# Optimization experiments

Measured on AMD Instinct MI355X. Metric: run time of the kernel, lower is better.

Reference implementation:

```python
import jax, jax.numpy as jnp
import numpy as np
import math

H = 16  # n_head
DK = 64  # d_k = n_feat // n_head
BASE = 10000.0


def _rope_cos_sin(T, dk, dtype):
    inv_freq = 1.0 / (BASE ** (jnp.arange(0, dk, 2, dtype=jnp.float32) / dk))
    t = jnp.arange(T, dtype=jnp.float32)
    freqs = jnp.einsum('i,j->ij', t, inv_freq)          # [T, dk/2]
    emb = jnp.concatenate([freqs, freqs], axis=-1)       # [T, dk]
    return jnp.cos(emb).astype(dtype)[:, None, None, :], jnp.sin(emb).astype(dtype)[:, None, None, :]


def _rotate_half(x):
    x1, x2 = jnp.split(x, 2, axis=-1)
    return jnp.concatenate([-x2, x1], axis=-1)


def setup_inputs() -> dict:
    key = jax.random.key(0)
    ks = jax.random.split(key, 8)
    T, B, C = 2048, 2, 1024
    s = 0.02
    return {
        'query': jax.random.normal(ks[0], (T, B, C), jnp.float32),
        'key': jax.random.normal(ks[1], (T, B, C), jnp.float32),
        'value': jax.random.normal(ks[2], (T, B, C), jnp.float32),
        'Wq': jax.random.normal(ks[3], (C, C), jnp.float32) * s,
        'bq': jnp.zeros((C,), jnp.float32),
        'Wk': jax.random.normal(ks[4], (C, C), jnp.float32) * s,
        'bk': jnp.zeros((C,), jnp.float32),
        'Wv': jax.random.normal(ks[5], (C, C), jnp.float32) * s,
        'bv': jnp.zeros((C,), jnp.float32),
        'Wo': jax.random.normal(ks[6], (C, C), jnp.float32) * s,
        'bo': jnp.zeros((C,), jnp.float32),
    }


def reference(query, key, value, Wq, bq, Wk, bk, Wv, bv, Wo, bo):
    T, B, C = value.shape
    # --- RoPE applied to raw inputs (per the original module), before projections ---
    q = query.reshape(T, B, H, DK)
    k = key.reshape(T, B, H, DK)
    cos, sin = _rope_cos_sin(T, DK, q.dtype)  # [T,1,1,DK]
    q = q * cos + _rotate_half(q) * sin
    k = k * cos + _rotate_half(k) * sin
    q = q.reshape(T, B, C).transpose(1, 0, 2)   # [B,T,C]
    k = k.reshape(T, B, C).transpose(1, 0, 2)
    v = value.transpose(1, 0, 2)
    # --- QKV projections (torch Linear: x @ W.T + b) ---
    q = (jnp.einsum('btc,dc->btd', q, Wq) + bq).reshape(B, T, H, DK).transpose(0, 2, 1, 3)
    k = (jnp.einsum('btc,dc->btd', k, Wk) + bk).reshape(B, T, H, DK).transpose(0, 2, 1, 3)
    v = (jnp.einsum('btc,dc->btd', v, Wv) + bv).reshape(B, T, H, DK).transpose(0, 2, 1, 3)
    # --- scaled dot-product attention ---
    scores = jnp.einsum('bhqd,bhkd->bhqk', q, k) / math.sqrt(DK)
    attn = jax.nn.softmax(scores, axis=-1)
    x = jnp.einsum('bhqk,bhkd->bhqd', attn, v)        # [B,H,T,DK]
    x = x.transpose(0, 2, 1, 3).reshape(B, T, C)
    out = jnp.einsum('btc,dc->btd', x, Wo) + bo        # [B,T,C]
    return out.transpose(1, 0, 2)                      # [T,B,C]
```

## Files before the change

### kernel.cpp

```cpp
#include <hip/hip_runtime.h>
#include <hip/hip_bf16.h>
#include <math.h>

#define T_SEQ 2048
#define B_SZ 2
#define C_DIM 1024
#define H_HEADS 16
#define DKH 64
#define M_ROWS (T_SEQ * B_SZ)

#define QSCALE 0.1803368801111204f

typedef __attribute__((ext_vector_type(8))) short bf16x8;
typedef __attribute__((ext_vector_type(4))) float f32x4;
typedef unsigned short ushort_t;


__device__ __forceinline__ ushort_t f2bf(float f) {
    unsigned u = __float_as_uint(f);
    u += 0x7fffu + ((u >> 16) & 1u);
    return (ushort_t)(u >> 16);
}

__device__ __forceinline__ unsigned pack2bf(float a, float b) {
#if __has_builtin(__builtin_amdgcn_cvt_pk_bf16_f32)
    typedef __attribute__((ext_vector_type(2))) __bf16 bf16x2_t;
    union { bf16x2_t v; unsigned u; } cv;
    cv.v = __builtin_amdgcn_cvt_pk_bf16_f32(a, b);
    return cv.u;
#else
    return (unsigned)f2bf(a) | ((unsigned)f2bf(b) << 16);
#endif
}

__device__ __forceinline__ void async_copy16(const void* g, void* l) {
    __builtin_amdgcn_global_load_lds(
        (const __attribute__((address_space(1))) void*)g,
        (__attribute__((address_space(3))) void*)l, 16, 0, 0);
}

__global__ __launch_bounds__(256) void prep_all(
        const float* __restrict__ q, const float* __restrict__ k,
        const float* __restrict__ value,
        const float* __restrict__ Wq, const float* __restrict__ Wk,
        const float* __restrict__ Wv, const float* __restrict__ Wo,
        ushort_t* __restrict__ qb, ushort_t* __restrict__ kb,
        ushort_t* __restrict__ vb2,
        ushort_t* __restrict__ Wqb, ushort_t* __restrict__ Wkb,
        ushort_t* __restrict__ Wvb, ushort_t* __restrict__ Wob) {
    int bid = blockIdx.x;
    int tid = threadIdx.x;
    if (bid < 8192) {
        int idx  = bid * 256 + tid;
        int j    = idx & 31;
        int rest = idx >> 5;
        int h    = rest & (H_HEADS - 1);
        int tb   = rest >> 4;
        int t    = tb >> 1;
        float inv = exp2f(-(float)j * 0.41524101186092034f);
        float ang = (float)t * inv;
        float s, c;
        sincosf(ang, &s, &c);
        int base = tb * C_DIM + h * DKH + j;
        float q1 = q[base], q2 = q[base + 32];
        float k1 = k[base], k2 = k[base + 32];
        qb[base]      = f2bf(q1 * c - q2 * s);
        qb[base + 32] = f2bf(q2 * c + q1 * s);
        kb[base]      = f2bf(k1 * c - k2 * s);
        kb[base + 32] = f2bf(k2 * c + k1 * s);
    } else if (bid < 12288) {
        int i   = (bid - 8192) * 256 + tid;
        int c4  = i & 255;
        int row = i >> 8;
        int b   = row >> 11, t = row & 2047;
        float4 v = reinterpret_cast<const float4*>(value)[(t * 2 + b) * 256 + c4];
        ushort4 o;
        o.x = f2bf(v.x); o.y = f2bf(v.y); o.z = f2bf(v.z); o.w = f2bf(v.w);
        reinterpret_cast<ushort4*>(vb2)[i] = o;
    } else {
        int r     = bid - 12288;
        int which = r >> 10;
        int i     = (r & 1023) * 256 + tid;
        const float* in = which == 0 ? Wq : which == 1 ? Wk : which == 2 ? Wv : Wo;
        ushort_t*   out = which == 0 ? Wqb : which == 1 ? Wkb : which == 2 ? Wvb : Wob;
        float4 v = reinterpret_cast<const float4*>(in)[i];
        ushort4 o;
        o.x = f2bf(v.x); o.y = f2bf(v.y); o.z = f2bf(v.z); o.w = f2bf(v.w);
        reinterpret_cast<ushort4*>(out)[i] = o;
    }
}

__device__ __forceinline__ void gemm_core(
        ushort_t* AsBase, ushort_t* BsBase,
        const ushort_t* __restrict__ A, const ushort_t* __restrict__ W,
        const float* __restrict__ bias, void* __restrict__ Cout,
        int N, int K, float scale, int rowBase, int colBase,
        bool biasRow, bool bf16out) {
    const int tid  = threadIdx.x;
    const int lane = tid & 63;
    const int w    = tid >> 6;
    const int m16  = lane & 15, quad = lane >> 4;
    const int r8   = lane >> 3, c8 = lane & 7;
    const int clog = c8 ^ r8;

    f32x4 acc[4];
#pragma unroll
    for (int j = 0; j < 4; j++) acc[j] = (f32x4){0.f, 0.f, 0.f, 0.f};

    auto stage = [&](int buf, int kt) {
#pragma unroll
        for (int i = 0; i < 2; ++i) {
            int R = w * 16 + i * 8;
            async_copy16(A + (size_t)(rowBase + R + r8) * K + kt + clog * 8,
                         AsBase + buf * 8192 + R * 64);
        }
        {
            int R = w * 8;
            async_copy16(W + (size_t)(colBase + R + r8) * K + kt + clog * 8,
                         BsBase + buf * 4096 + R * 64);
        }
    };

    stage(0, 0);
    int cur = 0;
    for (int kt = 0; kt < K; kt += 64, cur ^= 1) {
        if (kt + 64 < K) {
            stage(cur ^ 1, kt + 64);
            asm volatile("s_waitcnt vmcnt(3)" ::: "memory");
        } else {
            asm volatile("s_waitcnt vmcnt(0)" ::: "memory");
        }
        __builtin_amdgcn_s_barrier();
        __builtin_amdgcn_sched_barrier(0);
        const ushort_t* Asc = AsBase + cur * 8192;
        const ushort_t* Bsc = BsBase + cur * 4096;
#pragma unroll
        for (int ks = 0; ks < 2; ++ks) {
            int lc = ks * 4 + quad;
            bf16x8 af;
            {
                int R = w * 16 + m16;
                af = *reinterpret_cast<const bf16x8*>(
                    &Asc[R * 64 + ((lc ^ (R & 7)) << 3)]);
            }
            bf16x8 bfr[4];
#pragma unroll
            for (int ni = 0; ni < 4; ni++) {
                int R = ni * 16 + m16;
                bfr[ni] = *reinterpret_cast<const bf16x8*>(
                    &Bsc[R * 64 + ((lc ^ (R & 7)) << 3)]);
            }
#pragma unroll
            for (int ni = 0; ni < 4; ni++)
                acc[ni] = __builtin_amdgcn_mfma_f32_16x16x32_bf16(
                    af, bfr[ni], acc[ni], 0, 0, 0);
        }
        __builtin_amdgcn_s_barrier();
    }
#pragma unroll
    for (int ni = 0; ni < 4; ni++)
#pragma unroll
        for (int r = 0; r < 4; r++) {
            int row = rowBase + w * 16 + quad * 4 + r;
            int col = colBase + ni * 16 + m16;
            float v = (acc[ni][r] + (biasRow ? bias[row] : bias[col])) * scale;
            if (bf16out)
                ((ushort_t*)Cout)[(size_t)row * N + col] = f2bf(v);
            else
                ((float*)Cout)[(size_t)row * N + col] = v;
        }
}

__global__ __launch_bounds__(512) void qkv_gemm(
        const ushort_t* __restrict__ qb, const ushort_t* __restrict__ kb,
        const ushort_t* __restrict__ Wqb, const ushort_t* __restrict__ Wkb,
        const ushort_t* __restrict__ Wvb, const ushort_t* __restrict__ vb2,
        const float* __restrict__ bq, const float* __restrict__ bk,
        const float* __restrict__ bv,
        ushort_t* __restrict__ Qp, ushort_t* __restrict__ Kp,
        ushort_t* __restrict__ VTg) {
    __shared__ ushort_t As[2][128 * 64];
    __shared__ ushort_t Bs[2][64 * 64];
    int z = blockIdx.y;
    const ushort_t* A; const ushort_t* W; const float* bias; ushort_t* C;
    int N, bx, by; bool biasRow; float scale;
    if (z == 0) {
        A = qb;  W = Wqb; bias = bq; C = Qp;  N = C_DIM;  biasRow = false;
        scale = QSCALE; bx = blockIdx.x & 15; by = blockIdx.x >> 4;
    } else if (z == 1) {
        A = kb;  W = Wkb; bias = bk; C = Kp;  N = C_DIM;  biasRow = false;
        scale = 1.0f;   bx = blockIdx.x & 15; by = blockIdx.x >> 4;
    } else {
        A = Wvb; W = vb2; bias = bv; C = VTg; N = M_ROWS; biasRow = true;
        scale = 1.0f;   bx = blockIdx.x & 63; by = blockIdx.x >> 6;
    }
    gemm_core(&As[0][0], &Bs[0][0], A, W, bias, C, N, C_DIM, scale,
              by * 128, bx * 64, biasRow, true);
}

__global__ __launch_bounds__(512) void gemm_o(
        const ushort_t* __restrict__ Xb, const ushort_t* __restrict__ Wob,
        const float* __restrict__ bo, float* __restrict__ out) {
    __shared__ ushort_t As[2][128 * 64];
    __shared__ ushort_t Bs[2][64 * 64];
    gemm_core(&As[0][0], &Bs[0][0], Xb, Wob, bo, out, C_DIM, C_DIM, 1.0f,
              blockIdx.y * 128, blockIdx.x * 64, false, false);
}

__global__ __launch_bounds__(256) void attn(
        const ushort_t* __restrict__ Qp, const ushort_t* __restrict__ Kp,
        const ushort_t* __restrict__ VTg, ushort_t* __restrict__ X) {
    __shared__ char smem[40960];
    ushort_t* Qt = (ushort_t*)smem;
    char*  KtC   = smem + 8192;
    char*  VTC   = smem + 24576;
    float* exch  = (float*)(smem + 8192);
    float* lbuf  = (float*)smem;

    const int tid  = threadIdx.x;
    const int lane = tid & 63;
    const int w    = tid >> 6;
    const int m16  = lane & 15, quad = lane >> 4;
    const int r8   = lane >> 3, c8 = lane & 7;
    const int clog = c8 ^ r8;

    const int lid   = blockIdx.x + blockIdx.y * 32;
    const int jj    = lid >> 3;
    const int pair  = (lid & 7) * 4 + (jj >> 5);
    const int qBase = (jj & 31) * 64;
    const int b = pair >> 4, h = pair & 15;

    const int ofA = m16 * 128 + ((quad ^ (m16 & 7)) << 4);
    const int ofB = m16 * 128 + (((4 + quad) ^ (m16 & 7)) << 4);
    const int sw4 = (m16 >> 1) & 3;
    const int fro = m16 * 64 + ((quad ^ sw4) << 4);
    int pw0[2];
#pragma unroll
    for (int kt_i = 0; kt_i < 2; kt_i++)
        pw0[kt_i] = m16 * 64 + (((kt_i * 2 + (quad >> 1)) ^ sw4) << 4) + (quad & 1) * 8;
    char* PwC = KtC + w * 4096;

    const int vlc = (lane & 3) ^ ((lane >> 3) & 3);

#pragma unroll
    for (int i = 0; i < 2; ++i) {
        int R = w * 16 + i * 8;
        async_copy16(Qp + (size_t)((qBase + R + r8) * 2 + b) * C_DIM + h * DKH + clog * 8,
                     &Qt[R * 64]);
    }
    __syncthreads();
    bf16x8 aq[4][2];
#pragma unroll
    for (int ni = 0; ni < 4; ni++) {
        aq[ni][0] = *reinterpret_cast<const bf16x8*>((const char*)Qt + ni * 2048 + ofA);
        aq[ni][1] = *reinterpret_cast<const bf16x8*>((const char*)Qt + ni * 2048 + ofB);
    }
    asm volatile("s_waitcnt lgkmcnt(0)" ::: "memory");
    __syncthreads();

    float lrun[4] = {0.f, 0.f, 0.f, 0.f};
    f32x4 o[4][4];
#pragma unroll
    for (int mi = 0; mi < 4; mi++)
#pragma unroll
        for (int ni = 0; ni < 4; ni++) o[mi][ni] = (f32x4){0.f, 0.f, 0.f, 0.f};

    auto stageKV = [&](int kt) {
#pragma unroll
        for (int i = 0; i < 4; ++i) {
            int key = kt + w * 32 + i * 8 + r8;
            async_copy16(Kp + (size_t)(key * 2 + b) * C_DIM + h * DKH + clog * 8,
                         KtC + w * 4096 + i * 1024);
        }
#pragma unroll
        for (int i = 0; i < 4; ++i) {
            int dkr = i * 16 + (lane >> 2);
            async_copy16(VTg + (size_t)(h * DKH + dkr) * M_ROWS + b * T_SEQ + kt + w * 32 + vlc * 8,
                         VTC + w * 4096 + i * 1024);
        }
    };

    stageKV(0);
    for (int kt = 0; kt < T_SEQ; kt += 128) {
        asm volatile("s_waitcnt vmcnt(0)" ::: "memory");
        __builtin_amdgcn_sched_barrier(0);

        f32x4 s[2][4];
#pragma unroll
        for (int kt_i = 0; kt_i < 2; kt_i++) {
#pragma unroll
            for (int ni = 0; ni < 4; ni++) s[kt_i][ni] = (f32x4){0.f, 0.f, 0.f, 0.f};
            bf16x8 kf0 = *reinterpret_cast<const bf16x8*>(KtC + w * 4096 + kt_i * 2048 + ofA);
            bf16x8 kf1 = *reinterpret_cast<const bf16x8*>(KtC + w * 4096 + kt_i * 2048 + ofB);
#pragma unroll
            for (int ni = 0; ni < 4; ni++) {
                s[kt_i][ni] = __builtin_amdgcn_mfma_f32_16x16x32_bf16(kf0, aq[ni][0], s[kt_i][ni], 0, 0, 0);
                s[kt_i][ni] = __builtin_amdgcn_mfma_f32_16x16x32_bf16(kf1, aq[ni][1], s[kt_i][ni], 0, 0, 0);
            }
        }

#pragma unroll
        for (int kt_i = 0; kt_i < 2; kt_i++)
#pragma unroll
            for (int ni = 0; ni < 4; ni++) {
                float p0 = __builtin_amdgcn_exp2f(s[kt_i][ni][0]);
                float p1 = __builtin_amdgcn_exp2f(s[kt_i][ni][1]);
                float p2 = __builtin_amdgcn_exp2f(s[kt_i][ni][2]);
                float p3 = __builtin_amdgcn_exp2f(s[kt_i][ni][3]);
                lrun[ni] += (p0 + p1) + (p2 + p3);
                uint2 pv;
                pv.x = pack2bf(p0, p1);
                pv.y = pack2bf(p2, p3);
                *reinterpret_cast<uint2*>(PwC + ni * 1024 + pw0[kt_i]) = pv;
            }
        asm volatile("s_waitcnt lgkmcnt(0)" ::: "memory");

        bf16x8 pf[4];
#pragma unroll
        for (int ni = 0; ni < 4; ni++)
            pf[ni] = *reinterpret_cast<const bf16x8*>(PwC + ni * 1024 + fro);
        bf16x8 vfr[4];
#pragma unroll
        for (int mi = 0; mi < 4; mi++)
            vfr[mi] = *reinterpret_cast<const bf16x8*>(VTC + w * 4096 + mi * 1024 + fro);
        asm volatile("s_waitcnt lgkmcnt(0)" ::: "memory");
        __builtin_amdgcn_sched_barrier(0);
        if (kt + 128 < T_SEQ) stageKV(kt + 128);
        __builtin_amdgcn_sched_barrier(0);

#pragma unroll
        for (int mi = 0; mi < 4; mi++)
#pragma unroll
            for (int ni = 0; ni < 4; ni++)
                o[mi][ni] = __builtin_amdgcn_mfma_f32_16x16x32_bf16(vfr[mi], pf[ni], o[mi][ni], 0, 0, 0);
    }

#pragma unroll
    for (int ni = 0; ni < 4; ni++) {
        lrun[ni] += __shfl_xor(lrun[ni], 16);
        lrun[ni] += __shfl_xor(lrun[ni], 32);
    }
    float lv = quad == 0 ? lrun[0] : quad == 1 ? lrun[1] : quad == 2 ? lrun[2] : lrun[3];
    lbuf[w * 64 + quad * 16 + m16] = lv;

    __syncthreads();

#pragma unroll
    for (int rnd = 0; rnd < 2; rnd++) {
        if (rnd) __syncthreads();
#pragma unroll
        for (int t2 = 0; t2 < 2; t2++) {
            int mi = 2 * rnd + t2;
#pragma unroll
            for (int ni = 0; ni < 4; ni++) {
                int q = ni * 16 + m16;
                int cw = t2 * 4 + quad;
                *reinterpret_cast<f32x4*>(
                    &exch[w * 2048 + q * 32 + ((cw ^ (q & 7)) << 2)]) = o[mi][ni];
            }
        }
        __syncthreads();
        int q = tid >> 2;
        float lsum = lbuf[q] + lbuf[64 + q] + lbuf[128 + q] + lbuf[192 + q];
        float invl = 1.0f / lsum;
#pragma unroll
        for (int half = 0; half < 2; half++) {
            int c = (tid & 3) + 4 * half;
            int off = q * 32 + (((c ^ (q & 7))) << 2);
            f32x4 v = *reinterpret_cast<const f32x4*>(&exch[off]);
            f32x4 v1 = *reinterpret_cast<const f32x4*>(&exch[2048 + off]);
            f32x4 v2 = *reinterpret_cast<const f32x4*>(&exch[4096 + off]);
            f32x4 v3 = *reinterpret_cast<const f32x4*>(&exch[6144 + off]);
            v = v + v1 + v2 + v3;
            uint2 pk;
            pk.x = pack2bf(v[0] * invl, v[1] * invl);
            pk.y = pack2bf(v[2] * invl, v[3] * invl);
            int t = qBase + q;
            *reinterpret_cast<uint2*>(
                &X[(size_t)(t * 2 + b) * C_DIM + h * DKH + rnd * 32 + c * 4]) = pk;
        }
    }
}

extern "C" void kernel_launch(void* const* d_in, const int* in_sizes, int n_in,
                              void* d_out, int out_size, void* d_ws, size_t ws_size,
                              hipStream_t stream) {
    const float* query = (const float*)d_in[0];
    const float* key   = (const float*)d_in[1];
    const float* value = (const float*)d_in[2];
    const float* Wq = (const float*)d_in[3];
    const float* bq = (const float*)d_in[4];
    const float* Wk = (const float*)d_in[5];
    const float* bk = (const float*)d_in[6];
    const float* Wv = (const float*)d_in[7];
    const float* bv = (const float*)d_in[8];
    const float* Wo = (const float*)d_in[9];
    const float* bo = (const float*)d_in[10];
    float* out = (float*)d_out;

    ushort_t* qb  = (ushort_t*)d_ws;
    ushort_t* kb  = qb  + (size_t)M_ROWS * C_DIM;
    ushort_t* vb2 = kb  + (size_t)M_ROWS * C_DIM;
    ushort_t* Wqb = vb2 + (size_t)M_ROWS * C_DIM;
    ushort_t* Wkb = Wqb + (size_t)C_DIM * C_DIM;
    ushort_t* Wvb = Wkb + (size_t)C_DIM * C_DIM;
    ushort_t* Wob = Wvb + (size_t)C_DIM * C_DIM;
    ushort_t* Qp  = Wob + (size_t)C_DIM * C_DIM;
    ushort_t* Kp  = Qp  + (size_t)M_ROWS * C_DIM;
    ushort_t* VTg = Kp  + (size_t)M_ROWS * C_DIM;
    ushort_t* Xb  = VTg + (size_t)M_ROWS * C_DIM;

    prep_all<<<16384, 256, 0, stream>>>(query, key, value, Wq, Wk, Wv, Wo,
                                        qb, kb, vb2, Wqb, Wkb, Wvb, Wob);

    qkv_gemm<<<dim3(512, 3), 512, 0, stream>>>(qb, kb, Wqb, Wkb, Wvb, vb2,
                                               bq, bk, bv, Qp, Kp, VTg);

    attn<<<dim3(T_SEQ / 64, B_SZ * H_HEADS), 256, 0, stream>>>(Qp, Kp, VTg, Xb);

    gemm_o<<<dim3(C_DIM / 64, M_ROWS / 128), 512, 0, stream>>>(Xb, Wob, bo, out);
}
```

Measured before the change: 225.6 us.

## Switch GEMMs to 128x128 tiles with 4x4 MFMA per wave, drop double buffering

The shared GEMM core now uses 256-thread blocks computing 128x128 output tiles, where each wave computes a 64x64 sub-tile with a 4x4 grid of MFMA accumulators. Before, 512-thread blocks produced 128x64 tiles. Each fragment loaded from LDS now feeds more MFMAs, which raises data reuse and cuts global and LDS traffic per flop. In exchange, the async double-buffered prefetch is replaced by a single buffer with __syncthreads, so load latency is no longer overlapped with compute. The grids also shrink by half, which may reduce occupancy on a large GPU.

```diff
diff --git a/kernel.cpp b/kernel.cpp
--- a/kernel.cpp
+++ b/kernel.cpp
@@ -91,7 +91,7 @@
 }
 
 __device__ __forceinline__ void gemm_core(
-        ushort_t* AsBase, ushort_t* BsBase,
+        ushort_t* As, ushort_t* Bs,
         const ushort_t* __restrict__ A, const ushort_t* __restrict__ W,
         const float* __restrict__ bias, void* __restrict__ Cout,
         int N, int K, float scale, int rowBase, int colBase,
@@ -99,79 +99,75 @@
     const int tid  = threadIdx.x;
     const int lane = tid & 63;
     const int w    = tid >> 6;
+    const int wr   = (w >> 1) * 64;
+    const int wc   = (w & 1) * 64;
     const int m16  = lane & 15, quad = lane >> 4;
     const int r8   = lane >> 3, c8 = lane & 7;
     const int clog = c8 ^ r8;
 
-    f32x4 acc[4];
-#pragma unroll
-    for (int j = 0; j < 4; j++) acc[j] = (f32x4){0.f, 0.f, 0.f, 0.f};
-
-    auto stage = [&](int buf, int kt) {
-#pragma unroll
-        for (int i = 0; i < 2; ++i) {
-            int R = w * 16 + i * 8;
+    f32x4 acc[4][4];
+#pragma unroll
+    for (int mi = 0; mi < 4; mi++)
+#pragma unroll
+        for (int ni = 0; ni < 4; ni++) acc[mi][ni] = (f32x4){0.f, 0.f, 0.f, 0.f};
+
+    for (int kt = 0; kt < K; kt += 64) {
+#pragma unroll
+        for (int i = 0; i < 4; ++i) {
+            int R = w * 32 + i * 8;
             async_copy16(A + (size_t)(rowBase + R + r8) * K + kt + clog * 8,
-                         AsBase + buf * 8192 + R * 64);
-        }
-        {
-            int R = w * 8;
+                         As + R * 64);
+        }
+#pragma unroll
+        for (int i = 0; i < 4; ++i) {
+            int R = w * 32 + i * 8;
             async_copy16(W + (size_t)(colBase + R + r8) * K + kt + clog * 8,
-                         BsBase + buf * 4096 + R * 64);
-        }
-    };
-
-    stage(0, 0);
-    int cur = 0;
-    for (int kt = 0; kt < K; kt += 64, cur ^= 1) {
-        if (kt + 64 < K) {
-            stage(cur ^ 1, kt + 64);
-            asm volatile("s_waitcnt vmcnt(3)" ::: "memory");
-        } else {
-            asm volatile("s_waitcnt vmcnt(0)" ::: "memory");
-        }
-        __builtin_amdgcn_s_barrier();
-        __builtin_amdgcn_sched_barrier(0);
-        const ushort_t* Asc = AsBase + cur * 8192;
-        const ushort_t* Bsc = BsBase + cur * 4096;
+                         Bs + R * 64);
+        }
+        __syncthreads();
 #pragma unroll
         for (int ks = 0; ks < 2; ++ks) {
             int lc = ks * 4 + quad;
-            bf16x8 af;
-            {
-                int R = w * 16 + m16;
-                af = *reinterpret_cast<const bf16x8*>(
-                    &Asc[R * 64 + ((lc ^ (R & 7)) << 3)]);
+            bf16x8 af[4];
+#pragma unroll
+            for (int mi = 0; mi < 4; mi++) {
+                int R = wr + mi * 16 + m16;
+                af[mi] = *reinterpret_cast<const bf16x8*>(
+                    &As[R * 64 + ((lc ^ (R & 7)) << 3)]);
             }
             bf16x8 bfr[4];
 #pragma unroll
             for (int ni = 0; ni < 4; ni++) {
-                int R = ni * 16 + m16;
+                int R = wc + ni * 16 + m16;
                 bfr[ni] = *reinterpret_cast<const bf16x8*>(
-                    &Bsc[R * 64 + ((lc ^ (R & 7)) << 3)]);
-            }
-#pragma unroll
-            for (int ni = 0; ni < 4; ni++)
-                acc[ni] = __builtin_amdgcn_mfma_f32_16x16x32_bf16(
-                    af, bfr[ni], acc[ni], 0, 0, 0);
-        }
-        __builtin_amdgcn_s_barrier();
-    }
-#pragma unroll
-    for (int ni = 0; ni < 4; ni++)
-#pragma unroll
-        for (int r = 0; r < 4; r++) {
-            int row = rowBase + w * 16 + quad * 4 + r;
-            int col = colBase + ni * 16 + m16;
-            float v = (acc[ni][r] + (biasRow ? bias[row] : bias[col])) * scale;
-            if (bf16out)
-                ((ushort_t*)Cout)[(size_t)row * N + col] = f2bf(v);
-            else
-                ((float*)Cout)[(size_t)row * N + col] = v;
-        }
-}
-
-__global__ __launch_bounds__(512) void qkv_gemm(
+                    &Bs[R * 64 + ((lc ^ (R & 7)) << 3)]);
+            }
+#pragma unroll
+            for (int mi = 0; mi < 4; mi++)
+#pragma unroll
+                for (int ni = 0; ni < 4; ni++)
+                    acc[mi][ni] = __builtin_amdgcn_mfma_f32_16x16x32_bf16(
+                        af[mi], bfr[ni], acc[mi][ni], 0, 0, 0);
+        }
+        __syncthreads();
+    }
+#pragma unroll
+    for (int mi = 0; mi < 4; mi++)
+#pragma unroll
+        for (int ni = 0; ni < 4; ni++)
+#pragma unroll
+            for (int r = 0; r < 4; r++) {
+                int row = rowBase + wr + mi * 16 + quad * 4 + r;
+                int col = colBase + wc + ni * 16 + m16;
+                float v = (acc[mi][ni][r] + (biasRow ? bias[row] : bias[col])) * scale;
+                if (bf16out)
+                    ((ushort_t*)Cout)[(size_t)row * N + col] = f2bf(v);
+                else
+                    ((float*)Cout)[(size_t)row * N + col] = v;
+            }
+}
+
+__global__ __launch_bounds__(256) void qkv_gemm(
         const ushort_t* __restrict__ qb, const ushort_t* __restrict__ kb,
         const ushort_t* __restrict__ Wqb, const ushort_t* __restrict__ Wkb,
         const ushort_t* __restrict__ Wvb, const ushort_t* __restrict__ vb2,
@@ -179,32 +175,32 @@
         const float* __restrict__ bv,
         ushort_t* __restrict__ Qp, ushort_t* __restrict__ Kp,
         ushort_t* __restrict__ VTg) {
-    __shared__ ushort_t As[2][128 * 64];
-    __shared__ ushort_t Bs[2][64 * 64];
+    __shared__ ushort_t As[128 * 64];
+    __shared__ ushort_t Bs[128 * 64];
     int z = blockIdx.y;
     const ushort_t* A; const ushort_t* W; const float* bias; ushort_t* C;
     int N, bx, by; bool biasRow; float scale;
     if (z == 0) {
         A = qb;  W = Wqb; bias = bq; C = Qp;  N = C_DIM;  biasRow = false;
-        scale = QSCALE; bx = blockIdx.x & 15; by = blockIdx.x >> 4;
+        scale = QSCALE; bx = blockIdx.x & 7;  by = blockIdx.x >> 3;
     } else if (z == 1) {
         A = kb;  W = Wkb; bias = bk; C = Kp;  N = C_DIM;  biasRow = false;
-        scale = 1.0f;   bx = blockIdx.x & 15; by = blockIdx.x >> 4;
+        scale = 1.0f;   bx = blockIdx.x & 7;  by = blockIdx.x >> 3;
     } else {
         A = Wvb; W = vb2; bias = bv; C = VTg; N = M_ROWS; biasRow = true;
-        scale = 1.0f;   bx = blockIdx.x & 63; by = blockIdx.x >> 6;
-    }
-    gemm_core(&As[0][0], &Bs[0][0], A, W, bias, C, N, C_DIM, scale,
-              by * 128, bx * 64, biasRow, true);
-}
-
-__global__ __launch_bounds__(512) void gemm_o(
+        scale = 1.0f;   bx = blockIdx.x & 31; by = blockIdx.x >> 5;
+    }
+    gemm_core(As, Bs, A, W, bias, C, N, C_DIM, scale,
+              by * 128, bx * 128, biasRow, true);
+}
+
+__global__ __launch_bounds__(256) void gemm_o(
         const ushort_t* __restrict__ Xb, const ushort_t* __restrict__ Wob,
         const float* __restrict__ bo, float* __restrict__ out) {
-    __shared__ ushort_t As[2][128 * 64];
-    __shared__ ushort_t Bs[2][64 * 64];
-    gemm_core(&As[0][0], &Bs[0][0], Xb, Wob, bo, out, C_DIM, C_DIM, 1.0f,
-              blockIdx.y * 128, blockIdx.x * 64, false, false);
+    __shared__ ushort_t As[128 * 64];
+    __shared__ ushort_t Bs[128 * 64];
+    gemm_core(As, Bs, Xb, Wob, bo, out, C_DIM, C_DIM, 1.0f,
+              blockIdx.y * 128, blockIdx.x * 128, false, false);
 }
 
 __global__ __launch_bounds__(256) void attn(
@@ -413,10 +409,10 @@
     prep_all<<<16384, 256, 0, stream>>>(query, key, value, Wq, Wk, Wv, Wo,
                                         qb, kb, vb2, Wqb, Wkb, Wvb, Wob);
 
-    qkv_gemm<<<dim3(512, 3), 512, 0, stream>>>(qb, kb, Wqb, Wkb, Wvb, vb2,
+    qkv_gemm<<<dim3(256, 3), 256, 0, stream>>>(qb, kb, Wqb, Wkb, Wvb, vb2,
                                                bq, bk, bv, Qp, Kp, VTg);
 
     attn<<<dim3(T_SEQ / 64, B_SZ * H_HEADS), 256, 0, stream>>>(Qp, Kp, VTg, Xb);
 
-    gemm_o<<<dim3(C_DIM / 64, M_ROWS / 128), 512, 0, stream>>>(Xb, Wob, bo, out);
-}
+    gemm_o<<<dim3(C_DIM / 128, M_ROWS / 128), 256, 0, stream>>>(Xb, Wob, bo, out);
+}
```

Result: slower. 238.5 us (+5.7%).

## Enlarge QKV GEMM tile to 256x64 and split K/V prefetch in attention

Applied to the files above, without the earlier changes.

The QKV projection GEMM now uses 256x64 block tiles, with eight waves arranged 4x2 and each wave computing a 64x32 sub-tile. The grid is halved to match. This raises operand reuse per LDS load but drops the double-buffered prefetch in favor of a single buffer with __syncthreads around each k-step, so global loads no longer overlap MFMA work. The shared gemm_core is inlined into gemm_o without functional change. In attention, K and V staging are split so the next V tile is issued right after the current V fragments are read, overlapping V loads with the QK^T and softmax phase.

```diff
diff --git a/kernel.cpp b/kernel.cpp
--- a/kernel.cpp
+++ b/kernel.cpp
@@ -90,87 +90,6 @@
     }
 }
 
-__device__ __forceinline__ void gemm_core(
-        ushort_t* AsBase, ushort_t* BsBase,
-        const ushort_t* __restrict__ A, const ushort_t* __restrict__ W,
-        const float* __restrict__ bias, void* __restrict__ Cout,
-        int N, int K, float scale, int rowBase, int colBase,
-        bool biasRow, bool bf16out) {
-    const int tid  = threadIdx.x;
-    const int lane = tid & 63;
-    const int w    = tid >> 6;
-    const int m16  = lane & 15, quad = lane >> 4;
-    const int r8   = lane >> 3, c8 = lane & 7;
-    const int clog = c8 ^ r8;
-
-    f32x4 acc[4];
-#pragma unroll
-    for (int j = 0; j < 4; j++) acc[j] = (f32x4){0.f, 0.f, 0.f, 0.f};
-
-    auto stage = [&](int buf, int kt) {
-#pragma unroll
-        for (int i = 0; i < 2; ++i) {
-            int R = w * 16 + i * 8;
-            async_copy16(A + (size_t)(rowBase + R + r8) * K + kt + clog * 8,
-                         AsBase + buf * 8192 + R * 64);
-        }
-        {
-            int R = w * 8;
-            async_copy16(W + (size_t)(colBase + R + r8) * K + kt + clog * 8,
-                         BsBase + buf * 4096 + R * 64);
-        }
-    };
-
-    stage(0, 0);
-    int cur = 0;
-    for (int kt = 0; kt < K; kt += 64, cur ^= 1) {
-        if (kt + 64 < K) {
-            stage(cur ^ 1, kt + 64);
-            asm volatile("s_waitcnt vmcnt(3)" ::: "memory");
-        } else {
-            asm volatile("s_waitcnt vmcnt(0)" ::: "memory");
-        }
-        __builtin_amdgcn_s_barrier();
-        __builtin_amdgcn_sched_barrier(0);
-        const ushort_t* Asc = AsBase + cur * 8192;
-        const ushort_t* Bsc = BsBase + cur * 4096;
-#pragma unroll
-        for (int ks = 0; ks < 2; ++ks) {
-            int lc = ks * 4 + quad;
-            bf16x8 af;
-            {
-                int R = w * 16 + m16;
-                af = *reinterpret_cast<const bf16x8*>(
-                    &Asc[R * 64 + ((lc ^ (R & 7)) << 3)]);
-            }
-            bf16x8 bfr[4];
-#pragma unroll
-            for (int ni = 0; ni < 4; ni++) {
-                int R = ni * 16 + m16;
-                bfr[ni] = *reinterpret_cast<const bf16x8*>(
-                    &Bsc[R * 64 + ((lc ^ (R & 7)) << 3)]);
-            }
-#pragma unroll
-            for (int ni = 0; ni < 4; ni++)
-                acc[ni] = __builtin_amdgcn_mfma_f32_16x16x32_bf16(
-                    af, bfr[ni], acc[ni], 0, 0, 0);
-        }
-        __builtin_amdgcn_s_barrier();
-    }
-#pragma unroll
-    for (int ni = 0; ni < 4; ni++)
-#pragma unroll
-        for (int r = 0; r < 4; r++) {
-            int row = rowBase + w * 16 + quad * 4 + r;
-            int col = colBase + ni * 16 + m16;
-            float v = (acc[ni][r] + (biasRow ? bias[row] : bias[col])) * scale;
-            if (bf16out)
-                ((ushort_t*)Cout)[(size_t)row * N + col] = f2bf(v);
-            else
-                ((float*)Cout)[(size_t)row * N + col] = v;
-        }
-}
-
 __global__ __launch_bounds__(512) void qkv_gemm(
         const ushort_t* __restrict__ qb, const ushort_t* __restrict__ kb,
         const ushort_t* __restrict__ Wqb, const ushort_t* __restrict__ Wkb,
@@ -179,8 +98,8 @@
         const float* __restrict__ bv,
         ushort_t* __restrict__ Qp, ushort_t* __restrict__ Kp,
         ushort_t* __restrict__ VTg) {
-    __shared__ ushort_t As[2][128 * 64];
-    __shared__ ushort_t Bs[2][64 * 64];
+    __shared__ ushort_t As[256 * 64];
+    __shared__ ushort_t Bs[64 * 64];
     int z = blockIdx.y;
     const ushort_t* A; const ushort_t* W; const float* bias; ushort_t* C;
     int N, bx, by; bool biasRow; float scale;
@@ -194,8 +113,74 @@
         A = Wvb; W = vb2; bias = bv; C = VTg; N = M_ROWS; biasRow = true;
         scale = 1.0f;   bx = blockIdx.x & 63; by = blockIdx.x >> 6;
     }
-    gemm_core(&As[0][0], &Bs[0][0], A, W, bias, C, N, C_DIM, scale,
-              by * 128, bx * 64, biasRow, true);
+    const int K = C_DIM;
+    const int tid  = threadIdx.x;
+    const int lane = tid & 63;
+    const int w    = tid >> 6;
+    const int wr   = (w >> 1) * 64;
+    const int wc   = (w & 1) * 32;
+    const int m16  = lane & 15, quad = lane >> 4;
+    const int r8   = lane >> 3, c8 = lane & 7;
+    const int clog = c8 ^ r8;
+    const int rowBase = by * 256;
+    const int colBase = bx * 64;
+
+    f32x4 acc[4][2];
+#pragma unroll
+    for (int mi = 0; mi < 4; mi++)
+#pragma unroll
+        for (int ni = 0; ni < 2; ni++) acc[mi][ni] = (f32x4){0.f, 0.f, 0.f, 0.f};
+
+    for (int kt = 0; kt < K; kt += 64) {
+#pragma unroll
+        for (int i = 0; i < 4; ++i) {
+            int R = w * 32 + i * 8;
+            async_copy16(A + (size_t)(rowBase + R + r8) * K + kt + clog * 8,
+                         As + R * 64);
+        }
+        {
+            int R = w * 8;
+            async_copy16(W + (size_t)(colBase + R + r8) * K + kt + clog * 8,
+                         Bs + R * 64);
+        }
+        __syncthreads();
+#pragma unroll
+        for (int ks = 0; ks < 2; ++ks) {
+            int lc = ks * 4 + quad;
+            bf16x8 af[4];
+#pragma unroll
+            for (int mi = 0; mi < 4; mi++) {
+                int R = wr + mi * 16 + m16;
+                af[mi] = *reinterpret_cast<const bf16x8*>(
+                    &As[R * 64 + ((lc ^ (R & 7)) << 3)]);
+            }
+            bf16x8 bfr[2];
+#pragma unroll
+            for (int ni = 0; ni < 2; ni++) {
+                int R = wc + ni * 16 + m16;
+                bfr[ni] = *reinterpret_cast<const bf16x8*>(
+                    &Bs[R * 64 + ((lc ^ (R & 7)) << 3)]);
+            }
+#pragma unroll
+            for (int mi = 0; mi < 4; mi++)
+#pragma unroll
+                for (int ni = 0; ni < 2; ni++)
+                    acc[mi][ni] = __builtin_amdgcn_mfma_f32_16x16x32_bf16(
+                        af[mi], bfr[ni], acc[mi][ni], 0, 0, 0);
+        }
+        __syncthreads();
+    }
+#pragma unroll
+    for (int mi = 0; mi < 4; mi++)
+#pragma unroll
+        for (int ni = 0; ni < 2; ni++)
+#pragma unroll
+            for (int r = 0; r < 4; r++) {
+                int row = rowBase + wr + mi * 16 + quad * 4 + r;
+                int col = colBase + wc + ni * 16 + m16;
+                float v = (acc[mi][ni][r] + (biasRow ? bias[row] : bias[col])) * scale;
+                C[(size_t)row * N + col] = f2bf(v);
+            }
 }
 
 __global__ __launch_bounds__(512) void gemm_o(
@@ -203,8 +188,78 @@
         const float* __restrict__ bo, float* __restrict__ out) {
     __shared__ ushort_t As[2][128 * 64];
     __shared__ ushort_t Bs[2][64 * 64];
-    gemm_core(&As[0][0], &Bs[0][0], Xb, Wob, bo, out, C_DIM, C_DIM, 1.0f,
-              blockIdx.y * 128, blockIdx.x * 64, false, false);
+    const int K = C_DIM, N = C_DIM;
+    const int tid  = threadIdx.x;
+    const int lane = tid & 63;
+    const int w    = tid >> 6;
+    const int m16  = lane & 15, quad = lane >> 4;
+    const int r8   = lane >> 3, c8 = lane & 7;
+    const int clog = c8 ^ r8;
+    const int rowBase = blockIdx.y * 128;
+    const int colBase = blockIdx.x * 64;
+
+    f32x4 acc[4];
+#pragma unroll
+    for (int j = 0; j < 4; j++) acc[j] = (f32x4){0.f, 0.f, 0.f, 0.f};
+
+    auto stage = [&](int buf, int kt) {
+#pragma unroll
+        for (int i = 0; i < 2; ++i) {
+            int R = w * 16 + i * 8;
+            async_copy16(Xb + (size_t)(rowBase + R + r8) * K + kt + clog * 8,
+                         &As[buf][R * 64]);
+        }
+        {
+            int R = w * 8;
+            async_copy16(Wob + (size_t)(colBase + R + r8) * K + kt + clog * 8,
+                         &Bs[buf][R * 64]);
+        }
+    };
+
+    stage(0, 0);
+    int cur = 0;
+    for (int kt = 0; kt < K; kt += 64, cur ^= 1) {
+        if (kt + 64 < K) {
+            stage(cur ^ 1, kt + 64);
+            asm volatile("s_waitcnt vmcnt(3)" ::: "memory");
+        } else {
+            asm volatile("s_waitcnt vmcnt(0)" ::: "memory");
+        }
+        __builtin_amdgcn_s_barrier();
+        __builtin_amdgcn_sched_barrier(0);
+        const ushort_t* Asc = As[cur];
+        const ushort_t* Bsc = Bs[cur];
+#pragma unroll
+        for (int ks = 0; ks < 2; ++ks) {
+            int lc = ks * 4 + quad;
+            bf16x8 af;
+            {
+                int R = w * 16 + m16;
+                af = *reinterpret_cast<const bf16x8*>(
+                    &Asc[R * 64 + ((lc ^ (R & 7)) << 3)]);
+            }
+            bf16x8 bfr[4];
+#pragma unroll
+            for (int ni = 0; ni < 4; ni++) {
+                int R = ni * 16 + m16;
+                bfr[ni] = *reinterpret_cast<const bf16x8*>(
+                    &Bsc[R * 64 + ((lc ^ (R & 7)) << 3)]);
+            }
+#pragma unroll
+            for (int ni = 0; ni < 4; ni++)
+                acc[ni] = __builtin_amdgcn_mfma_f32_16x16x32_bf16(
+                    af, bfr[ni], acc[ni], 0, 0, 0);
+        }
+        __builtin_amdgcn_s_barrier();
+    }
+#pragma unroll
+    for (int ni = 0; ni < 4; ni++)
+#pragma unroll
+        for (int r = 0; r < 4; r++) {
+            int row = rowBase + w * 16 + quad * 4 + r;
+            int col = colBase + ni * 16 + m16;
+            out[(size_t)row * N + col] = acc[ni][r] + bo[col];
+        }
 }
 
 __global__ __launch_bounds__(256) void attn(
@@ -265,13 +320,15 @@
 #pragma unroll
         for (int ni = 0; ni < 4; ni++) o[mi][ni] = (f32x4){0.f, 0.f, 0.f, 0.f};
 
-    auto stageKV = [&](int kt) {
+    auto stageK = [&](int kt) {
 #pragma unroll
         for (int i = 0; i < 4; ++i) {
             int key = kt + w * 32 + i * 8 + r8;
             async_copy16(Kp + (size_t)(key * 2 + b) * C_DIM + h * DKH + clog * 8,
                          KtC + w * 4096 + i * 1024);
         }
+    };
+    auto stageV = [&](int kt) {
 #pragma unroll
         for (int i = 0; i < 4; ++i) {
             int dkr = i * 16 + (lane >> 2);
@@ -280,10 +337,18 @@
         }
     };
 
-    stageKV(0);
+    stageK(0); stageV(0);
     for (int kt = 0; kt < T_SEQ; kt += 128) {
         asm volatile("s_waitcnt vmcnt(0)" ::: "memory");
         __builtin_amdgcn_sched_barrier(0);
+
+        bf16x8 vfr[4];
+#pragma unroll
+        for (int mi = 0; mi < 4; mi++)
+            vfr[mi] = *reinterpret_cast<const bf16x8*>(VTC + w * 4096 + mi * 1024 + fro);
+        asm volatile("s_waitcnt lgkmcnt(0)" ::: "memory");
+        __builtin_amdgcn_sched_barrier(0);
+        if (kt + 128 < T_SEQ) stageV(kt + 128);
 
         f32x4 s[2][4];
 #pragma unroll
@@ -319,13 +384,9 @@
 #pragma unroll
         for (int ni = 0; ni < 4; ni++)
             pf[ni] = *reinterpret_cast<const bf16x8*>(PwC + ni * 1024 + fro);
-        bf16x8 vfr[4];
-#pragma unroll
-        for (int mi = 0; mi < 4; mi++)
-            vfr[mi] = *reinterpret_cast<const bf16x8*>(VTC + w * 4096 + mi * 1024 + fro);
         asm volatile("s_waitcnt lgkmcnt(0)" ::: "memory");
         __builtin_amdgcn_sched_barrier(0);
-        if (kt + 128 < T_SEQ) stageKV(kt + 128);
+        if (kt + 128 < T_SEQ) stageK(kt + 128);
         __builtin_amdgcn_sched_barrier(0);
 
 #pragma unroll
@@ -413,7 +474,7 @@
     prep_all<<<16384, 256, 0, stream>>>(query, key, value, Wq, Wk, Wv, Wo,
                                         qb, kb, vb2, Wqb, Wkb, Wvb, Wob);
 
-    qkv_gemm<<<dim3(512, 3), 512, 0, stream>>>(qb, kb, Wqb, Wkb, Wvb, vb2,
+    qkv_gemm<<<dim3(256, 3), 512, 0, stream>>>(qb, kb, Wqb, Wkb, Wvb, vb2,
                                                bq, bk, bv, Qp, Kp, VTg);
 
     attn<<<dim3(T_SEQ / 64, B_SZ * H_HEADS), 256, 0, stream>>>(Qp, Kp, VTg, Xb);
```

Measured after the change: 229.6 us. About the same (+1.8%).
